# Performance work log

Hardware: AMD Instinct MI355X
Metric: run time of the kernel (lower is better)

Reference implementation:

```python
import jax, jax.numpy as jnp
import numpy as np

E_INF = 1.5  # long-term modulus
E_MOD = 1.0  # Maxwell spring modulus
ETA = 2.0    # dashpot viscosity


def setup_inputs() -> dict:
    key = jax.random.key(0)
    k1, k2 = jax.random.split(key)
    B, T = 4096, 8192
    eps = jax.random.normal(k1, (B, T, 1), dtype=jnp.float32)          # strain history
    dt = jax.random.uniform(k2, (B, T, 1), dtype=jnp.float32)          # timestep sizes (>0)
    return {"eps": eps, "dt": dt}


def reference(eps, dt):
    # eps, dt: [B, T, 1]. Scan over time with internal variable gamma (state), gamma0 = 0.
    # Per step (matches MaxwellRNNCell.call):
    #   sig_n   = E_inf*eps_n + E*(eps_n - gamma_N)
    #   gamma_n = gamma_N + dt*(E/eta)*(eps_n - gamma_N)
    k = E_MOD / ETA
    eps_t = jnp.swapaxes(eps, 0, 1)  # [T, B, 1]
    dt_t = jnp.swapaxes(dt, 0, 1)    # [T, B, 1]

    def step(gamma, xs):
        e, d = xs
        diff = e - gamma
        sig = E_INF * e + E_MOD * diff
        gamma_new = gamma + d * k * diff
        return gamma_new, sig

    gamma0 = jnp.zeros((eps.shape[0], 1), dtype=eps.dtype)
    _, sig = jax.lax.scan(step, gamma0, (eps_t, dt_t))
    return jnp.swapaxes(sig, 0, 1)  # [B, T, 1]
```

## Files before the change

kernel.cpp:

```cpp
#include <hip/hip_runtime.h>


constexpr int   T_LEN   = 8192;
constexpr int   THREADS = 256;
constexpr int   V       = 8;
constexpr int   TILE    = THREADS * V;
constexpr int   NTILES  = T_LEN / TILE;
constexpr int   NWAVES  = THREADS / 64;
constexpr float KCOEF   = 0.5f;

__global__ __launch_bounds__(THREADS) void maxwell_scan_kernel(
    const float* __restrict__ eps, const float* __restrict__ dtv,
    float* __restrict__ out)
{
    const size_t row = (size_t)blockIdx.x * T_LEN;
    const float* e_row = eps + row;
    const float* d_row = dtv + row;
    float*       o_row = out + row;

    __shared__ float wA[NWAVES];
    __shared__ float wB[NWAVES];

    const int lane = threadIdx.x & 63;
    const int wid  = threadIdx.x >> 6;

    float gamma = 0.0f;

    for (int t = 0; t < NTILES; ++t) {
        const int base = t * TILE + threadIdx.x * V;

        float4 e0 = *(const float4*)(e_row + base);
        float4 e1 = *(const float4*)(e_row + base + 4);
        float4 d0 = *(const float4*)(d_row + base);
        float4 d1 = *(const float4*)(d_row + base + 4);
        float ev[V] = {e0.x, e0.y, e0.z, e0.w, e1.x, e1.y, e1.z, e1.w};
        float hv[V] = {d0.x * KCOEF, d0.y * KCOEF, d0.z * KCOEF, d0.w * KCOEF,
                       d1.x * KCOEF, d1.y * KCOEF, d1.z * KCOEF, d1.w * KCOEF};

        float A = 1.0f, Bc = 0.0f;
        #pragma unroll
        for (int j = 0; j < V; ++j) {
            float a = 1.0f - hv[j];
            Bc = a * Bc + hv[j] * ev[j];
            A  = a * A;
        }

        float sa = A, sb = Bc;
        #pragma unroll
        for (int off = 1; off < 64; off <<= 1) {
            float pa = __shfl_up(sa, off, 64);
            float pb = __shfl_up(sb, off, 64);
            if (lane >= off) {
                sb = sa * pb + sb;
                sa = sa * pa;
            }
        }
        if (lane == 63) { wA[wid] = sa; wB[wid] = sb; }
        __syncthreads();

        float ea = __shfl_up(sa, 1, 64);
        float eb = __shfl_up(sb, 1, 64);
        if (lane == 0) { ea = 1.0f; eb = 0.0f; }

        float pfa = 1.0f, pfb = 0.0f;
        float ta  = 1.0f, tb  = 0.0f;
        #pragma unroll
        for (int w = 0; w < NWAVES; ++w) {
            float a = wA[w], bb = wB[w];
            if (w < wid) { pfb = a * pfb + bb; pfa = a * pfa; }
            tb = a * tb + bb;
            ta = a * ta;
        }

        float xa = ea * pfa;
        float xb = ea * pfb + eb;
        float g  = xa * gamma + xb;

        float sg[V];
        #pragma unroll
        for (int j = 0; j < V; ++j) {
            sg[j] = 2.5f * ev[j] - g;
            g = g + hv[j] * (ev[j] - g);
        }
        *(float4*)(o_row + base)     = make_float4(sg[0], sg[1], sg[2], sg[3]);
        *(float4*)(o_row + base + 4) = make_float4(sg[4], sg[5], sg[6], sg[7]);

        gamma = ta * gamma + tb;
        __syncthreads();
    }
}

extern "C" void kernel_launch(void* const* d_in, const int* in_sizes, int n_in,
                              void* d_out, int out_size, void* d_ws, size_t ws_size,
                              hipStream_t stream) {
    const float* eps = (const float*)d_in[0];
    const float* dtv = (const float*)d_in[1];
    float* out = (float*)d_out;
    const int B = in_sizes[0] / T_LEN;
    maxwell_scan_kernel<<<B, THREADS, 0, stream>>>(eps, dtv, out);
}
```

Measured before the change: 307.8 us.

## Map one row per wavefront with register prefetch and nontemporal stores

Each wavefront now scans a whole row independently, removing the shared-memory cross-wave combine and both block barriers per tile. The next tile's inputs are prefetched into a register double buffer while the current tile is computed, and outputs use nontemporal stores. The costs are higher register use from 16 elements per lane plus the double buffer, and a strided per-lane access pattern.

```diff
diff --git a/kernel.cpp b/kernel.cpp
--- a/kernel.cpp
+++ b/kernel.cpp
@@ -1,92 +1,103 @@
 #include <hip/hip_runtime.h>
 
 
-constexpr int   T_LEN   = 8192;
-constexpr int   THREADS = 256;
-constexpr int   V       = 8;
-constexpr int   TILE    = THREADS * V;
-constexpr int   NTILES  = T_LEN / TILE;
-constexpr int   NWAVES  = THREADS / 64;
-constexpr float KCOEF   = 0.5f;
+typedef float fx4 __attribute__((ext_vector_type(4)));
 
-__global__ __launch_bounds__(THREADS) void maxwell_scan_kernel(
+constexpr int   T_LEN  = 8192;
+constexpr int   V      = 16;
+constexpr int   LTILE  = 64 * V;
+constexpr int   NT     = T_LEN / LTILE;
+constexpr int   WPB    = 4;
+constexpr int   THREADS = WPB * 64;
+constexpr float KCOEF  = 0.5f;
+
+__global__ __launch_bounds__(THREADS) void maxwell_wave_kernel(
     const float* __restrict__ eps, const float* __restrict__ dtv,
     float* __restrict__ out)
 {
-    const size_t row = (size_t)blockIdx.x * T_LEN;
+    const int lane   = threadIdx.x & 63;
+    const int wid    = threadIdx.x >> 6;
+    const int rowIdx = blockIdx.x * WPB + wid;
+    const size_t row = (size_t)rowIdx * T_LEN;
     const float* e_row = eps + row;
     const float* d_row = dtv + row;
     float*       o_row = out + row;
 
-    __shared__ float wA[NWAVES];
-    __shared__ float wB[NWAVES];
+    fx4 ebuf[2][4], dbuf[2][4];
 
-    const int lane = threadIdx.x & 63;
-    const int wid  = threadIdx.x >> 6;
+    {
+        const float* ep = e_row + lane * V;
+        const float* dp = d_row + lane * V;
+        #pragma unroll
+        for (int i = 0; i < 4; ++i) {
+            ebuf[0][i] = *(const fx4*)(ep + 4 * i);
+            dbuf[0][i] = *(const fx4*)(dp + 4 * i);
+        }
+    }
 
     float gamma = 0.0f;
 
-    for (int t = 0; t < NTILES; ++t) {
-        const int base = t * TILE + threadIdx.x * V;
+    for (int t = 0; t < NT; ++t) {
+        const int cur = t & 1, nxt = cur ^ 1;
 
-        float4 e0 = *(const float4*)(e_row + base);
-        float4 e1 = *(const float4*)(e_row + base + 4);
-        float4 d0 = *(const float4*)(d_row + base);
-        float4 d1 = *(const float4*)(d_row + base + 4);
-        float ev[V] = {e0.x, e0.y, e0.z, e0.w, e1.x, e1.y, e1.z, e1.w};
-        float hv[V] = {d0.x * KCOEF, d0.y * KCOEF, d0.z * KCOEF, d0.w * KCOEF,
-                       d1.x * KCOEF, d1.y * KCOEF, d1.z * KCOEF, d1.w * KCOEF};
+        if (t + 1 < NT) {
+            const float* ep = e_row + (t + 1) * LTILE + lane * V;
+            const float* dp = d_row + (t + 1) * LTILE + lane * V;
+            #pragma unroll
+            for (int i = 0; i < 4; ++i) {
+                ebuf[nxt][i] = *(const fx4*)(ep + 4 * i);
+                dbuf[nxt][i] = *(const fx4*)(dp + 4 * i);
+            }
+        }
+
+        float ev[V], hv[V];
+        #pragma unroll
+        for (int i = 0; i < 4; ++i) {
+            #pragma unroll
+            for (int j = 0; j < 4; ++j) {
+                ev[4*i+j] = ebuf[cur][i][j];
+                hv[4*i+j] = dbuf[cur][i][j] * KCOEF;
+            }
+        }
 
         float A = 1.0f, Bc = 0.0f;
         #pragma unroll
         for (int j = 0; j < V; ++j) {
-            float a = 1.0f - hv[j];
-            Bc = a * Bc + hv[j] * ev[j];
-            A  = a * A;
+            const float a = 1.0f - hv[j];
+            Bc = fmaf(a, Bc, hv[j] * ev[j]);
+            A *= a;
         }
 
         float sa = A, sb = Bc;
         #pragma unroll
         for (int off = 1; off < 64; off <<= 1) {
-            float pa = __shfl_up(sa, off, 64);
-            float pb = __shfl_up(sb, off, 64);
-            if (lane >= off) {
-                sb = sa * pb + sb;
-                sa = sa * pa;
-            }
+            const float pa = __shfl_up(sa, off, 64);
+            const float pb = __shfl_up(sb, off, 64);
+            if (lane >= off) { sb = fmaf(sa, pb, sb); sa *= pa; }
         }
-        if (lane == 63) { wA[wid] = sa; wB[wid] = sb; }
-        __syncthreads();
 
         float ea = __shfl_up(sa, 1, 64);
         float eb = __shfl_up(sb, 1, 64);
         if (lane == 0) { ea = 1.0f; eb = 0.0f; }
-
-        float pfa = 1.0f, pfb = 0.0f;
-        float ta  = 1.0f, tb  = 0.0f;
-        #pragma unroll
-        for (int w = 0; w < NWAVES; ++w) {
-            float a = wA[w], bb = wB[w];
-            if (w < wid) { pfb = a * pfb + bb; pfa = a * pfa; }
-            tb = a * tb + bb;
-            ta = a * ta;
-        }
-
-        float xa = ea * pfa;
-        float xb = ea * pfb + eb;
-        float g  = xa * gamma + xb;
+        float g = fmaf(ea, gamma, eb);
 
         float sg[V];
         #pragma unroll
         for (int j = 0; j < V; ++j) {
-            sg[j] = 2.5f * ev[j] - g;
-            g = g + hv[j] * (ev[j] - g);
+            sg[j] = fmaf(2.5f, ev[j], -g);
+            g = fmaf(hv[j], ev[j] - g, g);
         }
-        *(float4*)(o_row + base)     = make_float4(sg[0], sg[1], sg[2], sg[3]);
-        *(float4*)(o_row + base + 4) = make_float4(sg[4], sg[5], sg[6], sg[7]);
 
-        gamma = ta * gamma + tb;
-        __syncthreads();
+        float* op = o_row + t * LTILE + lane * V;
+        #pragma unroll
+        for (int i = 0; i < 4; ++i) {
+            fx4 s4 = {sg[4*i+0], sg[4*i+1], sg[4*i+2], sg[4*i+3]};
+            __builtin_nontemporal_store(s4, (fx4*)(op + 4 * i));
+        }
+
+        const float ta = __shfl(sa, 63, 64);
+        const float tb = __shfl(sb, 63, 64);
+        gamma = fmaf(ta, gamma, tb);
     }
 }
 
@@ -97,5 +108,5 @@
     const float* dtv = (const float*)d_in[1];
     float* out = (float*)d_out;
     const int B = in_sizes[0] / T_LEN;
-    maxwell_scan_kernel<<<B, THREADS, 0, stream>>>(eps, dtv, out);
+    maxwell_wave_kernel<<<B / WPB, THREADS, 0, stream>>>(eps, dtv, out);
 }
```

Measured after the change: 460.5 us. 49.6% more time.
